# Kernel optimization log

Hardware: AMD Instinct MI355X
Metric: run time of the kernel (lower is better)

Reference implementation:

```python
import jax, jax.numpy as jnp
import numpy as np

D_MODEL = 1024
NUM_HEADS = 16
D_K = D_MODEL // NUM_HEADS


def setup_inputs() -> dict:
    key = jax.random.key(0)
    ks = jax.random.split(key, 11)
    B, S, D = 2, 2048, D_MODEL
    scale = 1.0 / np.sqrt(D)
    inp = {
        'q': jax.random.normal(ks[0], (B, S, D), jnp.float32),
        'k': jax.random.normal(ks[1], (B, S, D), jnp.float32),
        'v': jax.random.normal(ks[2], (B, S, D), jnp.float32),
        'wq': jax.random.normal(ks[3], (D, D), jnp.float32) * scale,
        'bq': jnp.zeros((D,), jnp.float32),
        'wk': jax.random.normal(ks[4], (D, D), jnp.float32) * scale,
        'bk': jnp.zeros((D,), jnp.float32),
        'wv': jax.random.normal(ks[5], (D, D), jnp.float32) * scale,
        'bv': jnp.zeros((D,), jnp.float32),
        'wo': jax.random.normal(ks[6], (D, D), jnp.float32) * scale,
        'bo': jnp.zeros((D,), jnp.float32),
    }
    return inp


def _split_heads(x):
    B, S, _ = x.shape
    return x.reshape(B, S, NUM_HEADS, D_K).transpose(0, 2, 1, 3)  # [B,H,S,dk]


def reference(q, k, v, wq, bq, wk, bk, wv, bv, wo, bo):
    # Linear projections (torch Linear: x @ W^T + b)
    qh = _split_heads(q @ wq.T + bq)
    kh = _split_heads(k @ wk.T + bk)
    vh = _split_heads(v @ wv.T + bv)
    scores = jnp.einsum('bhqd,bhkd->bhqk', qh, kh) / np.sqrt(D_K)
    attn = jax.nn.softmax(scores, axis=-1)  # dropout is identity in eval
    ctx = jnp.einsum('bhqk,bhkd->bhqd', attn, vh)
    B, H, S, dk = ctx.shape
    ctx = ctx.transpose(0, 2, 1, 3).reshape(B, S, H * dk)
    return ctx @ wo.T + bo
```

## Files before the change

kernel.cpp:

```cpp
#include <hip/hip_runtime.h>
#include <hip/hip_bf16.h>
#include <math.h>

#define BATCH 2
#define SEQ   2048
#define DMODEL 1024
#define NHEAD 16
#define DK    64
#define M_TOT (BATCH*SEQ)
#define KDIM  DMODEL

typedef short bf16x8 __attribute__((ext_vector_type(8)));
typedef short bf16x4 __attribute__((ext_vector_type(4)));
typedef float f32x4  __attribute__((ext_vector_type(4)));
typedef __hip_bfloat16 bf16;

#define QSCALE 0.18033688011112042f

__device__ inline void gld_lds16(const void* g, void* l) {
    __builtin_amdgcn_global_load_lds(
        (const __attribute__((address_space(1))) unsigned int*)g,
        (__attribute__((address_space(3))) unsigned int*)l, 16, 0, 0);
}

__device__ inline unsigned pack2(float a, float b) {
    union { __hip_bfloat162 h; unsigned u; } t;
    t.h = __float22bfloat162_rn(make_float2(a, b));
    return t.u;
}

__global__ __launch_bounds__(256) void conv_inputs(
    const float* __restrict__ a, const float* __restrict__ b, const float* __restrict__ c,
    bf16* __restrict__ ah, bf16* __restrict__ bh, bf16* __restrict__ ch, int n)
{
    const float* src = blockIdx.y == 0 ? a : (blockIdx.y == 1 ? b : c);
    bf16* dst = blockIdx.y == 0 ? ah : (blockIdx.y == 1 ? bh : ch);
    const int i = (blockIdx.x * 256 + threadIdx.x) * 4;
    if (i < n) {
        float4 v = *(const float4*)(src + i);
        uint2 o;
        o.x = pack2(v.x, v.y);
        o.y = pack2(v.z, v.w);
        *(uint2*)(dst + i) = o;
    }
}

__global__ __launch_bounds__(256) void conv_weights(
    const float* __restrict__ wq, const float* __restrict__ wk,
    const float* __restrict__ wv, const float* __restrict__ wo,
    bf16* __restrict__ wqh, bf16* __restrict__ wkh, bf16* __restrict__ wvh,
    bf16* __restrict__ woh, bf16* __restrict__ wol, int n)
{
    const int t = blockIdx.y;
    const float* src = t == 0 ? wq : (t == 1 ? wk : (t == 2 ? wv : wo));
    bf16* dsth = t == 0 ? wqh : (t == 1 ? wkh : (t == 2 ? wvh : woh));
    const int i = (blockIdx.x * 256 + threadIdx.x) * 4;
    if (i >= n) return;
    float4 v = *(const float4*)(src + i);
    uint2 oh;
    oh.x = pack2(v.x, v.y);
    oh.y = pack2(v.z, v.w);
    *(uint2*)(dsth + i) = oh;
    if (t == 3) {
        float hx = __bfloat162float(__float2bfloat16(v.x));
        float hy = __bfloat162float(__float2bfloat16(v.y));
        float hz = __bfloat162float(__float2bfloat16(v.z));
        float hw = __bfloat162float(__float2bfloat16(v.w));
        uint2 ol;
        ol.x = pack2(v.x - hx, v.y - hy);
        ol.y = pack2(v.z - hz, v.w - hw);
        *(uint2*)(wol + i) = ol;
    }
}

template<int NSPLIT>
__device__ __forceinline__ void gemm_body(
    const bf16* __restrict__ Ah, const bf16* __restrict__ Al,
    const bf16* __restrict__ Wh, const bf16* __restrict__ Wl,
    const float* __restrict__ bias, void* __restrict__ out,
    int layout, float scale, bf16* sA, bf16* sB)
{
    const int tid  = threadIdx.x;
    const int wave = tid >> 6, lane = tid & 63;
    const int ln   = lane & 15, quad = lane >> 4;
    const int wm   = wave >> 1, wn = wave & 1;
    const int row0 = blockIdx.y * 128, col0 = blockIdx.x * 128;

    const int srow = lane >> 2;
    const int clog = (lane & 3) ^ (srow & 3);
    const size_t gA0 = (size_t)(row0 + wave * 16 + srow) * KDIM + clog * 8;
    const size_t gB0 = (size_t)(col0 + wave * 16 + srow) * KDIM + clog * 8;
    const int ldsoff = (wave * 16 + srow) * 64 + (lane & 3) * 16;

    const int swz = (quad ^ (ln & 3)) * 8;

    f32x4 acc[4][4] = {};

    for (int k0 = 0; k0 < KDIM; k0 += 32) {
        __syncthreads();
#pragma unroll
        for (int j = 0; j < 2; ++j) {
            const size_t go = (size_t)k0 + (size_t)j * 64 * KDIM;
            gld_lds16(Ah + gA0 + go, (char*)sA + j * 4096 + ldsoff);
            gld_lds16(Wh + gB0 + go, (char*)sB + j * 4096 + ldsoff);
            if (NSPLIT > 1) {
                gld_lds16(Al + gA0 + go, (char*)sA + 8192 + j * 4096 + ldsoff);
                gld_lds16(Wl + gB0 + go, (char*)sB + 8192 + j * 4096 + ldsoff);
            }
        }
        __syncthreads();

        bf16x8 af[4], bfr[4];
#pragma unroll
        for (int t = 0; t < 4; ++t) {
            af[t]  = *(const bf16x8*)&sA[(wm * 64 + t * 16 + ln) * 32 + swz];
            bfr[t] = *(const bf16x8*)&sB[(wn * 64 + t * 16 + ln) * 32 + swz];
        }
#pragma unroll
        for (int mt = 0; mt < 4; ++mt)
#pragma unroll
            for (int nt = 0; nt < 4; ++nt)
                acc[mt][nt] = __builtin_amdgcn_mfma_f32_16x16x32_bf16(af[mt], bfr[nt], acc[mt][nt], 0, 0, 0);

        if (NSPLIT > 1) {
            bf16x8 cf[4];
#pragma unroll
            for (int t = 0; t < 4; ++t)
                cf[t] = *(const bf16x8*)&sB[4096 + (wn * 64 + t * 16 + ln) * 32 + swz];
#pragma unroll
            for (int mt = 0; mt < 4; ++mt)
#pragma unroll
                for (int nt = 0; nt < 4; ++nt)
                    acc[mt][nt] = __builtin_amdgcn_mfma_f32_16x16x32_bf16(af[mt], cf[nt], acc[mt][nt], 0, 0, 0);
#pragma unroll
            for (int t = 0; t < 4; ++t)
                cf[t] = *(const bf16x8*)&sA[4096 + (wm * 64 + t * 16 + ln) * 32 + swz];
#pragma unroll
            for (int mt = 0; mt < 4; ++mt)
#pragma unroll
                for (int nt = 0; nt < 4; ++nt)
                    acc[mt][nt] = __builtin_amdgcn_mfma_f32_16x16x32_bf16(cf[mt], bfr[nt], acc[mt][nt], 0, 0, 0);
        }
    }

#pragma unroll
    for (int nt = 0; nt < 4; ++nt) {
        const int n = col0 + wn * 64 + nt * 16 + ln;
        const float bv = bias[n];
#pragma unroll
        for (int mt = 0; mt < 4; ++mt) {
#pragma unroll
            for (int r = 0; r < 4; ++r) {
                const int m = row0 + wm * 64 + mt * 16 + quad * 4 + r;
                const float v = (acc[mt][nt][r] + bv) * scale;
                if (layout == 0) {
                    ((float*)out)[(size_t)m * DMODEL + n] = v;
                } else {
                    const int b = m >> 11, s = m & (SEQ - 1);
                    const int h = n >> 6,  d = n & (DK - 1);
                    const int bh = b * NHEAD + h;
                    bf16 hv = __float2bfloat16(v);
                    if (layout == 1)
                        ((bf16*)out)[((size_t)bh * SEQ + s) * DK + d] = hv;
                    else
                        ((bf16*)out)[((size_t)bh * DK + d) * SEQ + s] = hv;
                }
            }
        }
    }
}

struct QKVArgs {
    const bf16* A[3];
    const bf16* W[3];
    const float* bias[3];
    bf16* out[3];
    float scale[3];
    int layout[3];
};

__global__ __launch_bounds__(256) void qkv_gemm(QKVArgs a) {
    __shared__ __align__(16) bf16 sA[128 * 32];
    __shared__ __align__(16) bf16 sB[128 * 32];
    const int z = blockIdx.z;
    gemm_body<1>(a.A[z], nullptr, a.W[z], nullptr, a.bias[z],
                 (void*)a.out[z], a.layout[z], a.scale[z], sA, sB);
}

__global__ __launch_bounds__(256) void gemm_o(
    const bf16* __restrict__ Ah, const bf16* __restrict__ Al,
    const bf16* __restrict__ Wh, const bf16* __restrict__ Wl,
    const float* __restrict__ bias, float* __restrict__ out)
{
    __shared__ __align__(16) bf16 sA[2 * 128 * 32];
    __shared__ __align__(16) bf16 sB[2 * 128 * 32];
    gemm_body<3>(Ah, Al, Wh, Wl, bias, (void*)out, 0, 1.0f, sA, sB);
}

#define NKT (SEQ / 64)
__global__ __launch_bounds__(256) void flash_attn_mfma(
    const bf16* __restrict__ Q, const bf16* __restrict__ K,
    const bf16* __restrict__ Vt,
    bf16* __restrict__ ctxh, bf16* __restrict__ ctxl)
{
    __shared__ __align__(16) bf16 Vts[64 * 64];

    const int tid  = threadIdx.x;
    const int wave = tid >> 6, lane = tid & 63;
    const int ln   = lane & 15, quad = lane >> 4;
    const int qt   = blockIdx.x;
    const int bh   = blockIdx.y;
    const int b    = bh >> 4, h = bh & (NHEAD - 1);

    const int q0 = qt * 128 + wave * 32;
    const bf16* Qb = Q + ((size_t)bh * SEQ + q0) * DK;
    bf16x8 qf[2][2];
#pragma unroll
    for (int c = 0; c < 2; ++c)
#pragma unroll
        for (int nt = 0; nt < 2; ++nt)
            qf[c][nt] = *(const bf16x8*)(Qb + (size_t)(nt * 16 + ln) * DK + c * 32 + quad * 8);

    f32x4 of[2][4] = {};
    float lp[2] = {0.f, 0.f};

    const int sr  = tid >> 2;
    const int scb = (tid & 3) * 2;
    const int ssw = sr & 7;
    const bf16* Vg0 = Vt + ((size_t)bh * DK + sr) * SEQ;
    const bf16* Kg0 = K + (size_t)bh * SEQ * DK;

    int vaddr[4];
#pragma unroll
    for (int mt = 0; mt < 4; ++mt)
        vaddr[mt] = ln * 64 + (((2 * mt + (quad >> 1)) ^ (ln & 7)) * 8) + (quad & 1) * 4;

    bf16x8 kfA[2][4], kfB[2][4];
    uint4 vA0, vA1, vB0, vB1;
#pragma unroll
    for (int c = 0; c < 2; ++c)
#pragma unroll
        for (int mt = 0; mt < 4; ++mt)
            kfA[c][mt] = *(const bf16x8*)(Kg0 + (size_t)(mt * 16 + ln) * DK + c * 32 + quad * 8);
    vA0 = *(const uint4*)(Vg0 + scb * 8);
    vA1 = *(const uint4*)(Vg0 + scb * 8 + 8);

    auto halfiter = [&](int ktc, bf16x8 (&kfc)[2][4], uint4& v0c, uint4& v1c,
                        bf16x8 (&kfn)[2][4], uint4& v0n, uint4& v1n) {
        __syncthreads();
        *(uint4*)(&Vts[sr * 64 + ((scb    ) ^ ssw) * 8]) = v0c;
        *(uint4*)(&Vts[sr * 64 + ((scb + 1) ^ ssw) * 8]) = v1c;
        __syncthreads();

        const int ktn = (ktc + 1) & (NKT - 1);
#pragma unroll
        for (int c = 0; c < 2; ++c)
#pragma unroll
            for (int mt = 0; mt < 4; ++mt)
                kfn[c][mt] = *(const bf16x8*)(Kg0 + (size_t)(ktn * 64 + mt * 16 + ln) * DK + c * 32 + quad * 8);
        v0n = *(const uint4*)(Vg0 + ktn * 64 + scb * 8);
        v1n = *(const uint4*)(Vg0 + ktn * 64 + scb * 8 + 8);

        f32x4 st[4][2] = {};
#pragma unroll
        for (int c = 0; c < 2; ++c)
#pragma unroll
            for (int mt = 0; mt < 4; ++mt)
#pragma unroll
                for (int nt = 0; nt < 2; ++nt)
                    st[mt][nt] = __builtin_amdgcn_mfma_f32_16x16x32_bf16(kfc[c][mt], qf[c][nt], st[mt][nt], 0, 0, 0);

        bf16x4 aP[4][2];
#pragma unroll
        for (int mt = 0; mt < 4; ++mt)
#pragma unroll
            for (int nt = 0; nt < 2; ++nt) {
                float p0 = __builtin_amdgcn_exp2f(st[mt][nt][0]);
                float p1 = __builtin_amdgcn_exp2f(st[mt][nt][1]);
                float p2 = __builtin_amdgcn_exp2f(st[mt][nt][2]);
                float p3 = __builtin_amdgcn_exp2f(st[mt][nt][3]);
                lp[nt] += (p0 + p1) + (p2 + p3);
                union { bf16x4 v; uint2 u; } uu;
                uu.u.x = pack2(p0, p1);
                uu.u.y = pack2(p2, p3);
                aP[mt][nt] = uu.v;
            }

#pragma unroll
        for (int mt = 0; mt < 4; ++mt)
#pragma unroll
            for (int ntd = 0; ntd < 4; ++ntd) {
                bf16x4 vf = *(const bf16x4*)(&Vts[vaddr[mt] + ntd * 1024]);
                of[0][ntd] = __builtin_amdgcn_mfma_f32_16x16x16bf16_1k(aP[mt][0], vf, of[0][ntd], 0, 0, 0);
                of[1][ntd] = __builtin_amdgcn_mfma_f32_16x16x16bf16_1k(aP[mt][1], vf, of[1][ntd], 0, 0, 0);
            }
    };

    for (int kt = 0; kt < NKT; kt += 2) {
        halfiter(kt,     kfA, vA0, vA1, kfB, vB0, vB1);
        halfiter(kt + 1, kfB, vB0, vB1, kfA, vA0, vA1);
    }

#pragma unroll
    for (int nt = 0; nt < 2; ++nt) {
        lp[nt] += __shfl_xor(lp[nt], 16, 64);
        lp[nt] += __shfl_xor(lp[nt], 32, 64);
    }
    float linv[2][4];
#pragma unroll
    for (int mtP = 0; mtP < 2; ++mtP)
#pragma unroll
        for (int r = 0; r < 4; ++r)
            linv[mtP][r] = 1.0f / __shfl(lp[mtP], quad * 4 + r, 64);

    const size_t base = ((size_t)b * SEQ + q0) * DMODEL + h * DK;
#pragma unroll
    for (int mtP = 0; mtP < 2; ++mtP)
#pragma unroll
        for (int nt = 0; nt < 4; ++nt)
#pragma unroll
            for (int r = 0; r < 4; ++r) {
                const float v = of[mtP][nt][r] * linv[mtP][r];
                const size_t idx = base + (size_t)(mtP * 16 + quad * 4 + r) * DMODEL + nt * 16 + ln;
                bf16 hv = __float2bfloat16(v);
                ctxh[idx] = hv;
                ctxl[idx] = __float2bfloat16(v - __bfloat162float(hv));
            }
}

extern "C" void kernel_launch(void* const* d_in, const int* in_sizes, int n_in,
                              void* d_out, int out_size, void* d_ws, size_t ws_size,
                              hipStream_t stream) {
    const float* q  = (const float*)d_in[0];
    const float* k  = (const float*)d_in[1];
    const float* v  = (const float*)d_in[2];
    const float* wq = (const float*)d_in[3];
    const float* bq = (const float*)d_in[4];
    const float* wk = (const float*)d_in[5];
    const float* bk = (const float*)d_in[6];
    const float* wv = (const float*)d_in[7];
    const float* bv = (const float*)d_in[8];
    const float* wo = (const float*)d_in[9];
    const float* bo = (const float*)d_in[10];
    float* out = (float*)d_out;

    char* ws = (char*)d_ws;
    const size_t MB = 1u << 20;
    bf16* q_hi  = (bf16*)(ws + 0 * MB);
    bf16* k_hi  = (bf16*)(ws + 8 * MB);
    bf16* v_hi  = (bf16*)(ws + 16 * MB);
    bf16* wq_hi = (bf16*)(ws + 24 * MB);
    bf16* wk_hi = (bf16*)(ws + 26 * MB);
    bf16* wv_hi = (bf16*)(ws + 28 * MB);
    bf16* wo_hi = (bf16*)(ws + 30 * MB);
    bf16* wo_lo = (bf16*)(ws + 32 * MB);
    bf16* Qp    = (bf16*)(ws + 34 * MB);
    bf16* Kp    = (bf16*)(ws + 42 * MB);
    bf16* Vpt   = (bf16*)(ws + 50 * MB);
    bf16* ctx_h = (bf16*)(ws + 0 * MB);
    bf16* ctx_l = (bf16*)(ws + 8 * MB);

    const int NX = M_TOT * DMODEL;
    const int NW = DMODEL * DMODEL;

    conv_inputs<<<dim3(NX / 1024, 3), 256, 0, stream>>>(q, k, v, q_hi, k_hi, v_hi, NX);
    conv_weights<<<dim3(NW / 1024, 4), 256, 0, stream>>>(wq, wk, wv, wo,
                                                          wq_hi, wk_hi, wv_hi, wo_hi, wo_lo, NW);

    QKVArgs qa;
    qa.A[0] = q_hi;  qa.A[1] = k_hi;  qa.A[2] = v_hi;
    qa.W[0] = wq_hi; qa.W[1] = wk_hi; qa.W[2] = wv_hi;
    qa.bias[0] = bq; qa.bias[1] = bk; qa.bias[2] = bv;
    qa.out[0] = Qp;  qa.out[1] = Kp;  qa.out[2] = Vpt;
    qa.scale[0] = QSCALE; qa.scale[1] = 1.0f; qa.scale[2] = 1.0f;
    qa.layout[0] = 1; qa.layout[1] = 1; qa.layout[2] = 2;

    dim3 qgrid(DMODEL / 128, M_TOT / 128, 3);
    qkv_gemm<<<qgrid, 256, 0, stream>>>(qa);

    dim3 fgrid(SEQ / 128, BATCH * NHEAD);
    flash_attn_mfma<<<fgrid, 256, 0, stream>>>(Qp, Kp, Vpt, ctx_h, ctx_l);

    dim3 ogrid(DMODEL / 128, M_TOT / 128);
    gemm_o<<<ogrid, 256, 0, stream>>>(ctx_h, ctx_l, wo_hi, wo_lo, bo, out);
}
```

Baseline: 276.7 us.

## Merge conversion kernels, split-K output GEMM, single-wave flash attention blocks

Fuses the input and weight conversion kernels into one launch. Splits the output projection GEMM into two K-halves that write fp32 partials, then adds them together with the bias in a new combine kernel, which doubles the number of output-GEMM blocks. Restructures flash attention into 64-thread single-wave blocks with 32 query rows each. V fragments are now read straight from global memory instead of being staged through LDS with barriers. The costs are extra partial-sum traffic, one more launch, and uncoalesced per-lane V loads.

```diff
diff --git a/kernel.cpp b/kernel.cpp
--- a/kernel.cpp
+++ b/kernel.cpp
@@ -29,47 +29,44 @@
     return t.u;
 }
 
-__global__ __launch_bounds__(256) void conv_inputs(
-    const float* __restrict__ a, const float* __restrict__ b, const float* __restrict__ c,
-    bf16* __restrict__ ah, bf16* __restrict__ bh, bf16* __restrict__ ch, int n)
-{
-    const float* src = blockIdx.y == 0 ? a : (blockIdx.y == 1 ? b : c);
-    bf16* dst = blockIdx.y == 0 ? ah : (blockIdx.y == 1 ? bh : ch);
-    const int i = (blockIdx.x * 256 + threadIdx.x) * 4;
-    if (i < n) {
-        float4 v = *(const float4*)(src + i);
-        uint2 o;
-        o.x = pack2(v.x, v.y);
-        o.y = pack2(v.z, v.w);
-        *(uint2*)(dst + i) = o;
-    }
-}
-
-__global__ __launch_bounds__(256) void conv_weights(
+__global__ __launch_bounds__(256) void conv_all(
+    const float* __restrict__ q, const float* __restrict__ k, const float* __restrict__ v,
     const float* __restrict__ wq, const float* __restrict__ wk,
     const float* __restrict__ wv, const float* __restrict__ wo,
+    bf16* __restrict__ qh, bf16* __restrict__ kh, bf16* __restrict__ vh,
     bf16* __restrict__ wqh, bf16* __restrict__ wkh, bf16* __restrict__ wvh,
-    bf16* __restrict__ woh, bf16* __restrict__ wol, int n)
-{
-    const int t = blockIdx.y;
-    const float* src = t == 0 ? wq : (t == 1 ? wk : (t == 2 ? wv : wo));
-    bf16* dsth = t == 0 ? wqh : (t == 1 ? wkh : (t == 2 ? wvh : woh));
+    bf16* __restrict__ woh, bf16* __restrict__ wol)
+{
+    const int y = blockIdx.y;
     const int i = (blockIdx.x * 256 + threadIdx.x) * 4;
-    if (i >= n) return;
-    float4 v = *(const float4*)(src + i);
-    uint2 oh;
-    oh.x = pack2(v.x, v.y);
-    oh.y = pack2(v.z, v.w);
-    *(uint2*)(dsth + i) = oh;
-    if (t == 3) {
-        float hx = __bfloat162float(__float2bfloat16(v.x));
-        float hy = __bfloat162float(__float2bfloat16(v.y));
-        float hz = __bfloat162float(__float2bfloat16(v.z));
-        float hw = __bfloat162float(__float2bfloat16(v.w));
-        uint2 ol;
-        ol.x = pack2(v.x - hx, v.y - hy);
-        ol.y = pack2(v.z - hz, v.w - hw);
-        *(uint2*)(wol + i) = ol;
+    if (y < 3) {
+        const float* src = y == 0 ? q : (y == 1 ? k : v);
+        bf16* dst = y == 0 ? qh : (y == 1 ? kh : vh);
+        float4 t = *(const float4*)(src + i);
+        uint2 o;
+        o.x = pack2(t.x, t.y);
+        o.y = pack2(t.z, t.w);
+        *(uint2*)(dst + i) = o;
+    } else {
+        const int w = i >> 20;
+        const int j = i & ((1 << 20) - 1);
+        const float* src = w == 0 ? wq : (w == 1 ? wk : (w == 2 ? wv : wo));
+        bf16* dsth = w == 0 ? wqh : (w == 1 ? wkh : (w == 2 ? wvh : woh));
+        float4 t = *(const float4*)(src + j);
+        uint2 oh;
+        oh.x = pack2(t.x, t.y);
+        oh.y = pack2(t.z, t.w);
+        *(uint2*)(dsth + j) = oh;
+        if (w == 3) {
+            float hx = __bfloat162float(__float2bfloat16(t.x));
+            float hy = __bfloat162float(__float2bfloat16(t.y));
+            float hz = __bfloat162float(__float2bfloat16(t.z));
+            float hw = __bfloat162float(__float2bfloat16(t.w));
+            uint2 ol;
+            ol.x = pack2(t.x - hx, t.y - hy);
+            ol.y = pack2(t.z - hz, t.w - hw);
+            *(uint2*)(wol + j) = ol;
+        }
     }
 }
 
@@ -78,7 +75,7 @@
     const bf16* __restrict__ Ah, const bf16* __restrict__ Al,
     const bf16* __restrict__ Wh, const bf16* __restrict__ Wl,
     const float* __restrict__ bias, void* __restrict__ out,
-    int layout, float scale, bf16* sA, bf16* sB)
+    int layout, float scale, bf16* sA, bf16* sB, int kb, int ke)
 {
     const int tid  = threadIdx.x;
     const int wave = tid >> 6, lane = tid & 63;
@@ -96,7 +93,7 @@
 
     f32x4 acc[4][4] = {};
 
-    for (int k0 = 0; k0 < KDIM; k0 += 32) {
+    for (int k0 = kb; k0 < ke; k0 += 32) {
         __syncthreads();
 #pragma unroll
         for (int j = 0; j < 2; ++j) {
@@ -146,14 +143,14 @@
 #pragma unroll
     for (int nt = 0; nt < 4; ++nt) {
         const int n = col0 + wn * 64 + nt * 16 + ln;
-        const float bv = bias[n];
+        const float bv = (layout == 3) ? 0.f : bias[n];
 #pragma unroll
         for (int mt = 0; mt < 4; ++mt) {
 #pragma unroll
             for (int r = 0; r < 4; ++r) {
                 const int m = row0 + wm * 64 + mt * 16 + quad * 4 + r;
                 const float v = (acc[mt][nt][r] + bv) * scale;
-                if (layout == 0) {
+                if (layout == 0 || layout == 3) {
                     ((float*)out)[(size_t)m * DMODEL + n] = v;
                 } else {
                     const int b = m >> 11, s = m & (SEQ - 1);
@@ -184,35 +181,50 @@
     __shared__ __align__(16) bf16 sB[128 * 32];
     const int z = blockIdx.z;
     gemm_body<1>(a.A[z], nullptr, a.W[z], nullptr, a.bias[z],
-                 (void*)a.out[z], a.layout[z], a.scale[z], sA, sB);
+                 (void*)a.out[z], a.layout[z], a.scale[z], sA, sB, 0, KDIM);
 }
 
 __global__ __launch_bounds__(256) void gemm_o(
     const bf16* __restrict__ Ah, const bf16* __restrict__ Al,
     const bf16* __restrict__ Wh, const bf16* __restrict__ Wl,
-    const float* __restrict__ bias, float* __restrict__ out)
+    float* __restrict__ p0, float* __restrict__ p1)
 {
     __shared__ __align__(16) bf16 sA[2 * 128 * 32];
     __shared__ __align__(16) bf16 sB[2 * 128 * 32];
-    gemm_body<3>(Ah, Al, Wh, Wl, bias, (void*)out, 0, 1.0f, sA, sB);
+    const int z = blockIdx.z;
+    gemm_body<3>(Ah, Al, Wh, Wl, nullptr, (void*)(z ? p1 : p0), 3, 1.0f,
+                 sA, sB, z * (KDIM / 2), (z + 1) * (KDIM / 2));
+}
+
+__global__ __launch_bounds__(256) void combine_o(
+    const float* __restrict__ p0, const float* __restrict__ p1,
+    const float* __restrict__ bias, float* __restrict__ out)
+{
+    const int i = (blockIdx.x * 256 + threadIdx.x) * 4;
+    float4 a = *(const float4*)(p0 + i);
+    float4 b = *(const float4*)(p1 + i);
+    float4 c = *(const float4*)(bias + (i & (DMODEL - 1)));
+    float4 o;
+    o.x = a.x + b.x + c.x;
+    o.y = a.y + b.y + c.y;
+    o.z = a.z + b.z + c.z;
+    o.w = a.w + b.w + c.w;
+    *(float4*)(out + i) = o;
 }
 
 #define NKT (SEQ / 64)
-__global__ __launch_bounds__(256) void flash_attn_mfma(
+__global__ __launch_bounds__(64, 2) void flash_attn_mfma(
     const bf16* __restrict__ Q, const bf16* __restrict__ K,
     const bf16* __restrict__ Vt,
     bf16* __restrict__ ctxh, bf16* __restrict__ ctxl)
 {
-    __shared__ __align__(16) bf16 Vts[64 * 64];
-
-    const int tid  = threadIdx.x;
-    const int wave = tid >> 6, lane = tid & 63;
+    const int lane = threadIdx.x;
     const int ln   = lane & 15, quad = lane >> 4;
     const int qt   = blockIdx.x;
     const int bh   = blockIdx.y;
     const int b    = bh >> 4, h = bh & (NHEAD - 1);
-
-    const int q0 = qt * 128 + wave * 32;
+    const int q0   = qt * 32;
+
     const bf16* Qb = Q + ((size_t)bh * SEQ + q0) * DK;
     bf16x8 qf[2][2];
 #pragma unroll
@@ -224,42 +236,30 @@
     f32x4 of[2][4] = {};
     float lp[2] = {0.f, 0.f};
 
-    const int sr  = tid >> 2;
-    const int scb = (tid & 3) * 2;
-    const int ssw = sr & 7;
-    const bf16* Vg0 = Vt + ((size_t)bh * DK + sr) * SEQ;
-    const bf16* Kg0 = K + (size_t)bh * SEQ * DK;
-
-    int vaddr[4];
-#pragma unroll
-    for (int mt = 0; mt < 4; ++mt)
-        vaddr[mt] = ln * 64 + (((2 * mt + (quad >> 1)) ^ (ln & 7)) * 8) + (quad & 1) * 4;
+    const bf16* Kl = K  + (size_t)bh * SEQ * DK + (size_t)ln * DK  + quad * 8;
+    const bf16* Vl = Vt + (size_t)bh * DK * SEQ + (size_t)ln * SEQ + quad * 4;
 
     bf16x8 kfA[2][4], kfB[2][4];
-    uint4 vA0, vA1, vB0, vB1;
 #pragma unroll
     for (int c = 0; c < 2; ++c)
 #pragma unroll
         for (int mt = 0; mt < 4; ++mt)
-            kfA[c][mt] = *(const bf16x8*)(Kg0 + (size_t)(mt * 16 + ln) * DK + c * 32 + quad * 8);
-    vA0 = *(const uint4*)(Vg0 + scb * 8);
-    vA1 = *(const uint4*)(Vg0 + scb * 8 + 8);
-
-    auto halfiter = [&](int ktc, bf16x8 (&kfc)[2][4], uint4& v0c, uint4& v1c,
-                        bf16x8 (&kfn)[2][4], uint4& v0n, uint4& v1n) {
-        __syncthreads();
-        *(uint4*)(&Vts[sr * 64 + ((scb    ) ^ ssw) * 8]) = v0c;
-        *(uint4*)(&Vts[sr * 64 + ((scb + 1) ^ ssw) * 8]) = v1c;
-        __syncthreads();
+            kfA[c][mt] = *(const bf16x8*)(Kl + (size_t)(mt * 16) * DK + c * 32);
+
+    auto halfiter = [&](int ktc, bf16x8 (&kfc)[2][4], bf16x8 (&kfn)[2][4]) {
+        bf16x4 vf[4][4];
+#pragma unroll
+        for (int mt = 0; mt < 4; ++mt)
+#pragma unroll
+            for (int nt = 0; nt < 4; ++nt)
+                vf[mt][nt] = *(const bf16x4*)(Vl + (size_t)(nt * 16) * SEQ + ktc * 64 + mt * 16);
 
         const int ktn = (ktc + 1) & (NKT - 1);
 #pragma unroll
         for (int c = 0; c < 2; ++c)
 #pragma unroll
             for (int mt = 0; mt < 4; ++mt)
-                kfn[c][mt] = *(const bf16x8*)(Kg0 + (size_t)(ktn * 64 + mt * 16 + ln) * DK + c * 32 + quad * 8);
-        v0n = *(const uint4*)(Vg0 + ktn * 64 + scb * 8);
-        v1n = *(const uint4*)(Vg0 + ktn * 64 + scb * 8 + 8);
+                kfn[c][mt] = *(const bf16x8*)(Kl + (size_t)(ktn * 64 + mt * 16) * DK + c * 32);
 
         f32x4 st[4][2] = {};
 #pragma unroll
@@ -289,16 +289,15 @@
 #pragma unroll
         for (int mt = 0; mt < 4; ++mt)
 #pragma unroll
-            for (int ntd = 0; ntd < 4; ++ntd) {
-                bf16x4 vf = *(const bf16x4*)(&Vts[vaddr[mt] + ntd * 1024]);
-                of[0][ntd] = __builtin_amdgcn_mfma_f32_16x16x16bf16_1k(aP[mt][0], vf, of[0][ntd], 0, 0, 0);
-                of[1][ntd] = __builtin_amdgcn_mfma_f32_16x16x16bf16_1k(aP[mt][1], vf, of[1][ntd], 0, 0, 0);
+            for (int nt = 0; nt < 4; ++nt) {
+                of[0][nt] = __builtin_amdgcn_mfma_f32_16x16x16bf16_1k(aP[mt][0], vf[mt][nt], of[0][nt], 0, 0, 0);
+                of[1][nt] = __builtin_amdgcn_mfma_f32_16x16x16bf16_1k(aP[mt][1], vf[mt][nt], of[1][nt], 0, 0, 0);
             }
     };
 
     for (int kt = 0; kt < NKT; kt += 2) {
-        halfiter(kt,     kfA, vA0, vA1, kfB, vB0, vB1);
-        halfiter(kt + 1, kfB, vB0, vB1, kfA, vA0, vA1);
+        halfiter(kt,     kfA, kfB);
+        halfiter(kt + 1, kfB, kfA);
     }
 
 #pragma unroll
@@ -346,26 +345,27 @@
 
     char* ws = (char*)d_ws;
     const size_t MB = 1u << 20;
-    bf16* q_hi  = (bf16*)(ws + 0 * MB);
-    bf16* k_hi  = (bf16*)(ws + 8 * MB);
-    bf16* v_hi  = (bf16*)(ws + 16 * MB);
-    bf16* wq_hi = (bf16*)(ws + 24 * MB);
-    bf16* wk_hi = (bf16*)(ws + 26 * MB);
-    bf16* wv_hi = (bf16*)(ws + 28 * MB);
-    bf16* wo_hi = (bf16*)(ws + 30 * MB);
-    bf16* wo_lo = (bf16*)(ws + 32 * MB);
+    bf16* wq_hi = (bf16*)(ws + 0 * MB);
+    bf16* wk_hi = (bf16*)(ws + 2 * MB);
+    bf16* wv_hi = (bf16*)(ws + 4 * MB);
+    bf16* wo_hi = (bf16*)(ws + 6 * MB);
+    bf16* wo_lo = (bf16*)(ws + 8 * MB);
+    bf16* q_hi  = (bf16*)(ws + 10 * MB);
+    bf16* k_hi  = (bf16*)(ws + 18 * MB);
+    bf16* v_hi  = (bf16*)(ws + 26 * MB);
     bf16* Qp    = (bf16*)(ws + 34 * MB);
     bf16* Kp    = (bf16*)(ws + 42 * MB);
     bf16* Vpt   = (bf16*)(ws + 50 * MB);
-    bf16* ctx_h = (bf16*)(ws + 0 * MB);
-    bf16* ctx_l = (bf16*)(ws + 8 * MB);
+    bf16* ctx_h = (bf16*)(ws + 10 * MB);
+    bf16* ctx_l = (bf16*)(ws + 18 * MB);
+    float* p0   = (float*)(ws + 26 * MB);
+    float* p1   = (float*)(ws + 42 * MB);
 
     const int NX = M_TOT * DMODEL;
-    const int NW = DMODEL * DMODEL;
-
-    conv_inputs<<<dim3(NX / 1024, 3), 256, 0, stream>>>(q, k, v, q_hi, k_hi, v_hi, NX);
-    conv_weights<<<dim3(NW / 1024, 4), 256, 0, stream>>>(wq, wk, wv, wo,
-                                                          wq_hi, wk_hi, wv_hi, wo_hi, wo_lo, NW);
+
+    conv_all<<<dim3(NX / 1024, 4), 256, 0, stream>>>(
+        q, k, v, wq, wk, wv, wo,
+        q_hi, k_hi, v_hi, wq_hi, wk_hi, wv_hi, wo_hi, wo_lo);
 
     QKVArgs qa;
     qa.A[0] = q_hi;  qa.A[1] = k_hi;  qa.A[2] = v_hi;
@@ -378,9 +378,11 @@
     dim3 qgrid(DMODEL / 128, M_TOT / 128, 3);
     qkv_gemm<<<qgrid, 256, 0, stream>>>(qa);
 
-    dim3 fgrid(SEQ / 128, BATCH * NHEAD);
-    flash_attn_mfma<<<fgrid, 256, 0, stream>>>(Qp, Kp, Vpt, ctx_h, ctx_l);
-
-    dim3 ogrid(DMODEL / 128, M_TOT / 128);
-    gemm_o<<<ogrid, 256, 0, stream>>>(ctx_h, ctx_l, wo_hi, wo_lo, bo, out);
-}
+    dim3 fgrid(SEQ / 32, BATCH * NHEAD);
+    flash_attn_mfma<<<fgrid, 64, 0, stream>>>(Qp, Kp, Vpt, ctx_h, ctx_l);
+
+    dim3 ogrid(DMODEL / 128, M_TOT / 128, 2);
+    gemm_o<<<ogrid, 256, 0, stream>>>(ctx_h, ctx_l, wo_hi, wo_lo, p0, p1);
+
+    combine_o<<<NX / 1024, 256, 0, stream>>>(p0, p1, bo, out);
+}
```

Measured after the change: 375.7 us. +35.8%, slower.
